# Kernel tuning notes

Hardware: AMD Instinct MI355X
Metric: run time of the kernel (lower is better)

Reference implementation:

```python
import jax, jax.numpy as jnp
import numpy as np

B, N, D, C = 8, 128, 256, 3

def setup_inputs() -> dict:
    key = jax.random.key(0)
    k1, k2, k3, k4, k5 = jax.random.split(key, 5)
    s_v = jax.random.normal(k1, (B, N, D), dtype=jnp.float32)
    s_e = jax.random.normal(k2, (B, N, N, D), dtype=jnp.float32)
    sub_graph = jax.random.randint(k3, (B,), 0, N)
    s_e_score = jax.random.uniform(k4, (B, C, N), dtype=jnp.float32)
    # per-graph node counts in [1, N], float since used as divisor
    num_node = jax.random.randint(k5, (B,), 1, N + 1).astype(jnp.float32)
    return {"s_v": s_v, "s_e": s_e, "sub_graph": sub_graph,
            "s_e_score": s_e_score, "num_node": num_node}

def reference(s_v, s_e, sub_graph, s_e_score, num_node):
    b, n, d = s_v.shape
    score2 = s_e_score[:, :2]                                   # (B,2,N)
    lam_b = jnp.sum(score2.reshape(b, -1), axis=-1, keepdims=True) + 1e-6  # (B,1)
    zero_one_hot = jnp.ones((b, n), dtype=s_v.dtype).at[:, 0].set(0.0)
    sub_graph_mask = jax.nn.one_hot(sub_graph, n, dtype=s_v.dtype) * zero_one_hot  # (B,N)
    score = jnp.sum(score2, axis=1) + sub_graph_mask            # (B,N)
    lam = score / lam_b                                         # (B,N)
    # sum_{i,j} (s_v[i] + s_e[i,j]) * lam[i] == sum_i lam[i] * (N*s_v[i] + sum_j s_e[i,j])
    # -- identical math to the torch broadcast, without the (B,N,N,D) intermediate
    agg = n * s_v + jnp.sum(s_e, axis=2)                        # (B,N,D)
    r_G = jnp.einsum('bn,bnd->bd', lam, agg)                    # (B,D)
    r_G = r_G / (num_node[:, None] ** 2)
    return r_G[:, None, :]                                      # (B,1,D)
```

## Files before the change

### kernel.cpp

```cpp
#include <hip/hip_runtime.h>

#define BB 8
#define NN 128
#define DD 256
#define NF4 (DD / 4)

__global__ __launch_bounds__(256) void pass1_kernel(
    const float4* __restrict__ se4,
    const float4* __restrict__ sv4,
    const float*  __restrict__ se_score,
    const int*    __restrict__ sub_graph,
    const float*  __restrict__ num_node,
    float4* __restrict__ ws4)
{
    const int blk = blockIdx.x;
    const int b   = blk >> 7;
    const int n   = blk & 127;
    const int tid = threadIdx.x;
    const int v   = tid & 63;
    const int s   = tid >> 6;

    __shared__ float red[4];
    {
        float x = se_score[b * 3 * NN + tid];
        #pragma unroll
        for (int off = 32; off > 0; off >>= 1)
            x += __shfl_down(x, off, 64);
        if ((tid & 63) == 0) red[tid >> 6] = x;
    }
    __syncthreads();
    const float lam_b = red[0] + red[1] + red[2] + red[3] + 1e-6f;

    const float4* __restrict__ p = se4 + (size_t)(b * NN + n) * (NN * NF4);

    float4 a0 = make_float4(0.f, 0.f, 0.f, 0.f);
    float4 a1 = make_float4(0.f, 0.f, 0.f, 0.f);
    #pragma unroll 4
    for (int m = s; m < NN; m += 8) {
        const float4 x = p[m * NF4 + v];
        const float4 y = p[(m + 4) * NF4 + v];
        a0.x += x.x; a0.y += x.y; a0.z += x.z; a0.w += x.w;
        a1.x += y.x; a1.y += y.y; a1.z += y.z; a1.w += y.w;
    }
    float4 a;
    a.x = a0.x + a1.x; a.y = a0.y + a1.y;
    a.z = a0.z + a1.z; a.w = a0.w + a1.w;

    __shared__ float4 sm[256];
    sm[tid] = a;
    __syncthreads();

    if (tid < 64) {
        const float4 t0 = sm[tid];
        const float4 t1 = sm[tid + 64];
        const float4 t2 = sm[tid + 128];
        const float4 t3 = sm[tid + 192];

        const float sc   = se_score[b * 3 * NN + n] + se_score[b * 3 * NN + NN + n];
        const float mask = (sub_graph[b] == n && n != 0) ? 1.0f : 0.0f;
        const float nnum = num_node[b];
        const float w    = (sc + mask) / (lam_b * nnum * nnum);

        const float4 sv = sv4[(size_t)(b * NN + n) * NF4 + v];

        float4 r;
        r.x = w * (128.0f * sv.x + t0.x + t1.x + t2.x + t3.x);
        r.y = w * (128.0f * sv.y + t0.y + t1.y + t2.y + t3.y);
        r.z = w * (128.0f * sv.z + t0.z + t1.z + t2.z + t3.z);
        r.w = w * (128.0f * sv.w + t0.w + t1.w + t2.w + t3.w);

        ws4[(size_t)(b * NN + n) * NF4 + v] = r;
    }
}

__global__ __launch_bounds__(256) void pass2_kernel(
    const float4* __restrict__ ws4,
    float4* __restrict__ out4)
{
    const int b    = blockIdx.x;
    const int tid  = threadIdx.x;
    const int v    = tid & 63;
    const int part = tid >> 6;

    const float4* __restrict__ p = ws4 + (size_t)b * NN * NF4;

    float4 a = make_float4(0.f, 0.f, 0.f, 0.f);
    #pragma unroll 8
    for (int n = part * 32; n < part * 32 + 32; ++n) {
        const float4 x = p[n * NF4 + v];
        a.x += x.x; a.y += x.y; a.z += x.z; a.w += x.w;
    }

    __shared__ float4 sm[256];
    sm[tid] = a;
    __syncthreads();

    if (tid < 64) {
        const float4 t0 = sm[tid];
        const float4 t1 = sm[tid + 64];
        const float4 t2 = sm[tid + 128];
        const float4 t3 = sm[tid + 192];
        float4 r;
        r.x = t0.x + t1.x + t2.x + t3.x;
        r.y = t0.y + t1.y + t2.y + t3.y;
        r.z = t0.z + t1.z + t2.z + t3.z;
        r.w = t0.w + t1.w + t2.w + t3.w;
        out4[b * NF4 + v] = r;
    }
}

extern "C" void kernel_launch(void* const* d_in, const int* in_sizes, int n_in,
                              void* d_out, int out_size, void* d_ws, size_t ws_size,
                              hipStream_t stream) {
    const float* s_v       = (const float*)d_in[0];
    const float* s_e       = (const float*)d_in[1];
    const int*   sub_graph = (const int*)  d_in[2];
    const float* s_e_score = (const float*)d_in[3];
    const float* num_node  = (const float*)d_in[4];
    float4* out4 = (float4*)d_out;
    float4* ws4  = (float4*)d_ws;

    pass1_kernel<<<BB * NN, 256, 0, stream>>>(
        (const float4*)s_e, (const float4*)s_v, s_e_score, sub_graph, num_node, ws4);
    pass2_kernel<<<BB, 256, 0, stream>>>(ws4, out4);
}
```

Measured before the change: 200.7 us.

## Split each node's edge reduction across two blocks and defer lam_b reduction

Pass 1 now launches twice as many blocks, each summing half of the neighbor dimension for a node, and writes two partial rows per node that pass 2 folds in. The lam_b reduction moves from a block-wide shuffle plus __syncthreads at kernel start to a single-wave float4 load and xor-shuffle done after the main streaming loop. This is meant to add memory-level parallelism and remove an early barrier from the bandwidth-bound read of s_e. The cost is a doubled workspace, more work in pass 2, and a redundant lam_b computation in every block.

```diff
diff --git a/kernel.cpp b/kernel.cpp
--- a/kernel.cpp
+++ b/kernel.cpp
@@ -14,29 +14,21 @@
     float4* __restrict__ ws4)
 {
     const int blk = blockIdx.x;
-    const int b   = blk >> 7;
-    const int n   = blk & 127;
+    const int b   = blk >> 8;
+    const int rr  = blk & 255;
+    const int n   = rr >> 1;
+    const int h   = rr & 1;
     const int tid = threadIdx.x;
     const int v   = tid & 63;
     const int s   = tid >> 6;
 
-    __shared__ float red[4];
-    {
-        float x = se_score[b * 3 * NN + tid];
-        #pragma unroll
-        for (int off = 32; off > 0; off >>= 1)
-            x += __shfl_down(x, off, 64);
-        if ((tid & 63) == 0) red[tid >> 6] = x;
-    }
-    __syncthreads();
-    const float lam_b = red[0] + red[1] + red[2] + red[3] + 1e-6f;
-
-    const float4* __restrict__ p = se4 + (size_t)(b * NN + n) * (NN * NF4);
+    const float4* __restrict__ p =
+        se4 + ((size_t)(b * NN + n) * NN + h * 64) * NF4;
 
     float4 a0 = make_float4(0.f, 0.f, 0.f, 0.f);
     float4 a1 = make_float4(0.f, 0.f, 0.f, 0.f);
-    #pragma unroll 4
-    for (int m = s; m < NN; m += 8) {
+    #pragma unroll
+    for (int m = s; m < 64; m += 8) {
         const float4 x = p[m * NF4 + v];
         const float4 y = p[(m + 4) * NF4 + v];
         a0.x += x.x; a0.y += x.y; a0.z += x.z; a0.w += x.w;
@@ -56,20 +48,35 @@
         const float4 t2 = sm[tid + 128];
         const float4 t3 = sm[tid + 192];
 
+        const float4* __restrict__ sc4 =
+            (const float4*)(se_score + b * 3 * NN);
+        const float4 q = sc4[tid];
+        float lam = q.x + q.y + q.z + q.w;
+        #pragma unroll
+        for (int off = 32; off > 0; off >>= 1)
+            lam += __shfl_xor(lam, off, 64);
+        const float lam_b = lam + 1e-6f;
+
         const float sc   = se_score[b * 3 * NN + n] + se_score[b * 3 * NN + NN + n];
         const float mask = (sub_graph[b] == n && n != 0) ? 1.0f : 0.0f;
         const float nnum = num_node[b];
         const float w    = (sc + mask) / (lam_b * nnum * nnum);
 
-        const float4 sv = sv4[(size_t)(b * NN + n) * NF4 + v];
+        float4 r;
+        r.x = w * (t0.x + t1.x + t2.x + t3.x);
+        r.y = w * (t0.y + t1.y + t2.y + t3.y);
+        r.z = w * (t0.z + t1.z + t2.z + t3.z);
+        r.w = w * (t0.w + t1.w + t2.w + t3.w);
 
-        float4 r;
-        r.x = w * (128.0f * sv.x + t0.x + t1.x + t2.x + t3.x);
-        r.y = w * (128.0f * sv.y + t0.y + t1.y + t2.y + t3.y);
-        r.z = w * (128.0f * sv.z + t0.z + t1.z + t2.z + t3.z);
-        r.w = w * (128.0f * sv.w + t0.w + t1.w + t2.w + t3.w);
+        if (h == 0) {
+            const float4 sv = sv4[(size_t)(b * NN + n) * NF4 + v];
+            r.x += w * 128.0f * sv.x;
+            r.y += w * 128.0f * sv.y;
+            r.z += w * 128.0f * sv.z;
+            r.w += w * 128.0f * sv.w;
+        }
 
-        ws4[(size_t)(b * NN + n) * NF4 + v] = r;
+        ws4[((size_t)(b * NN + n) * 2 + h) * NF4 + v] = r;
     }
 }
 
@@ -82,12 +89,12 @@
     const int v    = tid & 63;
     const int part = tid >> 6;
 
-    const float4* __restrict__ p = ws4 + (size_t)b * NN * NF4;
+    const float4* __restrict__ p = ws4 + (size_t)b * (NN * 2) * NF4;
 
     float4 a = make_float4(0.f, 0.f, 0.f, 0.f);
     #pragma unroll 8
-    for (int n = part * 32; n < part * 32 + 32; ++n) {
-        const float4 x = p[n * NF4 + v];
+    for (int r = part * 64; r < part * 64 + 64; ++r) {
+        const float4 x = p[r * NF4 + v];
         a.x += x.x; a.y += x.y; a.z += x.z; a.w += x.w;
     }
 
@@ -120,7 +127,7 @@
     float4* out4 = (float4*)d_out;
     float4* ws4  = (float4*)d_ws;
 
-    pass1_kernel<<<BB * NN, 256, 0, stream>>>(
+    pass1_kernel<<<2 * BB * NN, 256, 0, stream>>>(
         (const float4*)s_e, (const float4*)s_v, s_e_score, sub_graph, num_node, ws4);
     pass2_kernel<<<BB, 256, 0, stream>>>(ws4, out4);
 }
```

Result: no change. 202.8 us (+1.0%).
